# Performance work log

Measured on AMD Instinct MI355X. Metric: run time of the kernel, lower is better.

Reference implementation:

```python
import jax, jax.numpy as jnp
import numpy as np

S = 100                     # MC weight samples
B = 128                     # batch
CONV1 = (100, 20, 1, 5, 5)  # (S, Cout, Cin, kh, kw)
CONV2 = (100, 50, 20, 5, 5)
AFF1 = (100, 500, 800)      # (S, out, in)
AFF2 = (100, 10, 500)
W_OFF = np.cumsum([0, 500, 25000, 400000, 5000])
B_OFF = np.cumsum([0, 20, 50, 500, 10])
NW, NB = 430500, 580


def _softplus(r):
    return jnp.log1p(jnp.exp(r))  # sigma_T(rho) = log(1 + exp(rho))


def _conv(h, w, b):
    # h: (B, S or 1, Cin, H, W); w: (S, Cout, Cin, kh, kw); b: (S, Cout)
    def one(xs, ws):  # xs: (B,Cin,H,W), ws: (Cout,Cin,kh,kw)
        return jax.lax.conv_general_dilated(xs, ws, (1, 1), 'VALID')
    if h.shape[1] == 1:  # shared input broadcast over samples (first layer)
        out = jax.vmap(one, in_axes=(None, 0), out_axes=1)(h[:, 0], w)
    else:
        out = jax.vmap(one, in_axes=(1, 0), out_axes=1)(h, w)
    return out + b[None, :, :, None, None]  # (B,S,Cout,H',W')


def _maxpool(h):  # 2x2 stride-2 over trailing spatial dims
    return jax.lax.reduce_window(h, -jnp.inf, jax.lax.max,
                                 (1, 1, 1, 2, 2), (1, 1, 1, 2, 2), 'VALID')


def setup_inputs() -> dict:
    key = jax.random.key(0)
    ks = jax.random.split(key, 4)
    x = jax.random.normal(ks[0], (B, 1, 28, 28), dtype=jnp.float32)
    e = jax.random.normal(ks[1], (S, NW + NB), dtype=jnp.float32)
    mu_w = jax.random.normal(ks[2], (NW,), dtype=jnp.float32) * 0.05
    rho_w = jnp.ones((NW,), dtype=jnp.float32) * 0.5
    mu_b = jax.random.normal(ks[3], (NB,), dtype=jnp.float32) * 0.05
    rho_b = jnp.ones((NB,), dtype=jnp.float32) * 0.5
    return {"x": x, "e": e, "mu_w": mu_w, "rho_w": rho_w,
            "mu_b": mu_b, "rho_b": rho_b}


def reference(x, e, mu_w, rho_w, mu_b, rho_b):
    # reparameterized per-sample weights: (S, NW) and (S, NB)
    w = mu_w + _softplus(rho_w) * e[:, :NW]
    b = mu_b + _softplus(rho_b) * e[:, NW:]

    h = x[:, None]  # (B,1,1,28,28): singleton MC dim broadcasts
    # conv1 + relu + pool
    h = _conv(h, w[:, W_OFF[0]:W_OFF[1]].reshape(CONV1), b[:, B_OFF[0]:B_OFF[1]])
    h = _maxpool(jax.nn.relu(h))                     # (B,S,20,12,12)
    # conv2 + relu + pool
    h = _conv(h, w[:, W_OFF[1]:W_OFF[2]].reshape(CONV2), b[:, B_OFF[1]:B_OFF[2]])
    h = _maxpool(jax.nn.relu(h))                     # (B,S,50,4,4)
    h = h.reshape(h.shape[0], h.shape[1], -1)        # (B,S,800)
    # aff1 + relu
    w3 = w[:, W_OFF[2]:W_OFF[3]].reshape(AFF1)
    h = jax.nn.relu(jnp.einsum('bsi,soi->bso', h, w3) + b[None, :, B_OFF[2]:B_OFF[3]])
    # aff2 + log_softmax
    w4 = w[:, W_OFF[3]:W_OFF[4]].reshape(AFF2)
    h = jnp.einsum('bsi,soi->bso', h, w4) + b[None, :, B_OFF[3]:B_OFF[4]]
    h = jax.nn.log_softmax(h, axis=-1)               # (B,S,10)
    return h.mean(axis=1)                            # eval path: mean over MC samples
```

## Files before the change

kernel.cpp:

```cpp
#include <hip/hip_runtime.h>
#include <math.h>

#define Sn 100
#define Bn 128
#define NWc 430500
#define EWc 431080

typedef __attribute__((ext_vector_type(8)))  short bhalf8;
typedef __attribute__((ext_vector_type(16))) float fx16;

__device__ __forceinline__ float sp_f(float r){
    return fmaxf(r, 0.f) + log1pf(__expf(-fabsf(r)));
}
__device__ __forceinline__ ushort bfr(float f){
    union { float f; uint u; } c; c.f = f;
    uint r = (c.u + 0x7FFFu + ((c.u >> 16) & 1u)) >> 16;
    return (ushort)r;
}

__global__ void k00_sp(const float* __restrict__ rho_w, const float* __restrict__ rho_b,
                       float* __restrict__ sp_all){
    int i = blockIdx.x * blockDim.x + threadIdx.x;
    if (i < NWc)      sp_all[i] = sp_f(rho_w[i]);
    else if (i < EWc) sp_all[i] = sp_f(rho_b[i - NWc]);
}

__global__ __launch_bounds__(256) void k0_w3t(const float* __restrict__ e,
        const float* __restrict__ mu_w, const float* __restrict__ sp_all,
        ushort* __restrict__ w3){
    __shared__ __align__(16) ushort ls[20*808];
    int oc = blockIdx.x;
    int s  = blockIdx.y;
    int o0 = oc * 20;
    int tid = threadIdx.x;
    const float* eb = e + (size_t)s*EWc + 25500 + (size_t)o0*800;
    const float* mb = mu_w   + 25500 + (size_t)o0*800;
    const float* pb = sp_all + 25500 + (size_t)o0*800;
    #pragma unroll 4
    for (int j = tid; j < 4000; j += 256){
        int o = j / 200, k4 = j - o*200;
        float4 ev = *(const float4*)(eb + j*4);
        float4 mv = *(const float4*)(mb + j*4);
        float4 sv = *(const float4*)(pb + j*4);
        ushort4 t;
        t.x = bfr(fmaf(sv.x, ev.x, mv.x));
        t.y = bfr(fmaf(sv.y, ev.y, mv.y));
        t.z = bfr(fmaf(sv.z, ev.z, mv.z));
        t.w = bfr(fmaf(sv.w, ev.w, mv.w));
        *(ushort4*)&ls[o*808 + k4*4] = t;
    }
    __syncthreads();
    if (tid < 200){
        int kt = tid >> 3, l8 = tid & 7;
        ushort* wb = w3 + (size_t)s*400000 + kt*16000 + o0*32;
        #pragma unroll
        for (int it = 0; it < 10; ++it){
            int idx = it*8 + l8;
            int o = idx >> 2, kp = (idx & 3)*8;
            uint4 v = *(const uint4*)&ls[o*808 + kt*32 + kp];
            *(uint4*)(wb + idx*8) = v;
        }
    }
}

__global__ void k0_small(const float* __restrict__ e, const float* __restrict__ mu_w,
                       const float* __restrict__ sp_all, const float* __restrict__ mu_b,
                       float* __restrict__ w1, ushort* __restrict__ w2r,
                       float* __restrict__ w4, float* __restrict__ ball){
    const int per = 31080;
    int idx = blockIdx.x * blockDim.x + threadIdx.x;
    if (idx >= Sn * per) return;
    int s = idx / per, j = idx % per;
    if (j < 500){
        float v = fmaf(sp_all[j], e[(size_t)s*EWc + j], mu_w[j]);
        w1[s*500 + j] = v;
    } else if (j < 25500){
        int g = j;
        float v = fmaf(sp_all[g], e[(size_t)s*EWc + g], mu_w[g]);
        int j2 = j - 500;
        int oc = j2 / 500, rem = j2 % 500;
        int ic = rem / 25, kk = rem % 25;
        w2r[(size_t)s*51200 + (kk*64 + oc)*32 + ic] = bfr(v);
    } else if (j < 30500){
        int g = 425500 + (j - 25500);
        float v = fmaf(sp_all[g], e[(size_t)s*EWc + g], mu_w[g]);
        w4[s*5000 + (j - 25500)] = v;
    } else {
        int k = j - 30500;
        float v = fmaf(sp_all[NWc + k], e[(size_t)s*EWc + NWc + k], mu_b[k]);
        ball[s*580 + k] = v;
    }
}

__global__ __launch_bounds__(256, 2) void k1_conv1(const float* __restrict__ x,
        const float* __restrict__ w1, const float* __restrict__ ball,
        ushort* __restrict__ h1p){
    __shared__ __align__(16) float xs[784];
    __shared__ __align__(16) float w1s[500];
    __shared__ float b1s[20];
    __shared__ __align__(16) ushort ots[2880];
    int bid = blockIdx.x;
    int s = bid / Bn, b = bid % Bn;
    int tid = threadIdx.x;
    for (int i = tid; i < 784; i += 256) xs[i] = x[b*784 + i];
    for (int i = tid; i < 500; i += 256) w1s[i] = w1[s*500 + i];
    if (tid < 20) b1s[tid] = ball[s*580 + tid];
    __syncthreads();
    if (tid < 240){
        int c = tid / 12, y = tid % 12;

        float acc0[24], acc1[24];
        #pragma unroll
        for (int i = 0; i < 24; ++i){ acc0[i] = 0.f; acc1[i] = 0.f; }

        #pragma unroll
        for (int ky = 0; ky < 5; ++ky){
            float rlo[28], rhi[28];
            const float* plo = &xs[(2*y + ky) * 28];
            const float* phi = &xs[(2*y + ky + 1) * 28];
            #pragma unroll
            for (int cc = 0; cc < 28; cc += 4){
                float4 v0 = *(const float4*)(plo + cc);
                rlo[cc] = v0.x; rlo[cc+1] = v0.y; rlo[cc+2] = v0.z; rlo[cc+3] = v0.w;
                float4 v1 = *(const float4*)(phi + cc);
                rhi[cc] = v1.x; rhi[cc+1] = v1.y; rhi[cc+2] = v1.z; rhi[cc+3] = v1.w;
            }
            #pragma unroll
            for (int kx = 0; kx < 5; ++kx){
                float wv = w1s[c*25 + ky*5 + kx];
                #pragma unroll
                for (int cx = 0; cx < 24; ++cx){
                    acc0[cx] = fmaf(rlo[cx + kx], wv, acc0[cx]);
                    acc1[cx] = fmaf(rhi[cx + kx], wv, acc1[cx]);
                }
            }
        }
        float bias = b1s[c];
        #pragma unroll
        for (int px = 0; px < 12; ++px){
            float m = fmaxf(fmaxf(acc0[2*px], acc0[2*px+1]),
                            fmaxf(acc1[2*px], acc1[2*px+1]));
            ots[(y*12 + px)*20 + c] = bfr(fmaxf(m + bias, 0.f));
        }
    }
    __syncthreads();
    const uint* o32 = (const uint*)ots;
    uint* g32 = (uint*)(h1p + (s*Bn + b)*2880);
    for (int j = tid; j < 1440; j += 256) g32[j] = o32[j];
}

#define ICS 40
__global__ __launch_bounds__(256, 3) void k2_direct(const ushort* __restrict__ h1p,
        const ushort* __restrict__ w2r, const float* __restrict__ ball,
        ushort* __restrict__ h2p){
    __shared__ __align__(16) ushort img[4*144*ICS];
    int bid = blockIdx.x;
    int s = bid >> 5, g = bid & 31;
    int tid = threadIdx.x;
    const uint* g32 = (const uint*)(h1p + (size_t)(s*Bn + g*4)*2880);
    uint* l32 = (uint*)img;
    for (int j = tid; j < 5760; j += 256){
        int im = j / 1440, r = j - im*1440;
        int p = r / 10, u = r - p*10;
        l32[im*2880 + p*20 + u] = g32[j];
    }
    for (int j = tid; j < 3456; j += 256){
        int im = j / 864, r = j - im*864;
        int p = r / 6, u = 10 + (r - p*6);
        l32[im*2880 + p*20 + u] = 0u;
    }
    __syncthreads();

    int wv = tid >> 6, l = tid & 63;
    int l31 = l & 31, q = l >> 5;
    const ushort* imgw = img + wv*5760;
    int pixb0 = ((l31      ) >> 3)*12 + (l31 & 7);
    int pixb1 = ((l31 + 32 ) >> 3)*12 + (l31 & 7);
    const ushort* wb0 = w2r + (size_t)(s*25)*2048 + (l31     )*32;
    const ushort* wb1 = w2r + (size_t)(s*25)*2048 + (l31 + 32)*32;
    fx16 acc00 = (fx16)0.f, acc01 = (fx16)0.f, acc10 = (fx16)0.f, acc11 = (fx16)0.f;

    #pragma unroll 1
    for (int kk = 0; kk < 25; ++kk){
        int ky = kk / 5, kx = kk - ky*5;
        int poff = ky*12 + kx;
        #pragma unroll
        for (int ics = 0; ics < 2; ++ics){
            bhalf8 a0 = *(const bhalf8*)(imgw + (pixb0 + poff)*ICS + ics*16 + q*8);
            bhalf8 a1 = *(const bhalf8*)(imgw + (pixb1 + poff)*ICS + ics*16 + q*8);
            bhalf8 b0 = *(const bhalf8*)(wb0 + kk*2048 + ics*16 + q*8);
            bhalf8 b1 = *(const bhalf8*)(wb1 + kk*2048 + ics*16 + q*8);
            acc00 = __builtin_amdgcn_mfma_f32_32x32x16_bf16(a0, b0, acc00, 0, 0, 0);
            acc01 = __builtin_amdgcn_mfma_f32_32x32x16_bf16(a0, b1, acc01, 0, 0, 0);
            acc10 = __builtin_amdgcn_mfma_f32_32x32x16_bf16(a1, b0, acc10, 0, 0, 0);
            acc11 = __builtin_amdgcn_mfma_f32_32x32x16_bf16(a1, b1, acc11, 0, 0, 0);
        }
    }
    int b = g*4 + wv;
    ushort* dst = h2p + (size_t)s*102400 + (size_t)b*32;
    #pragma unroll
    for (int nt = 0; nt < 2; ++nt){
        int oc = nt*32 + l31;
        if (oc >= 50) continue;
        float bias = ball[s*580 + 20 + oc];
        #pragma unroll
        for (int mt = 0; mt < 2; ++mt){
            fx16 a;
            if (nt == 0) a = mt ? acc10 : acc00;
            else         a = mt ? acc11 : acc01;
            #pragma unroll
            for (int gp = 0; gp < 2; ++gp){
                float p0 = fmaxf(fmaxf(a[8*gp+0], a[8*gp+1]), fmaxf(a[8*gp+4], a[8*gp+5]));
                float p1 = fmaxf(fmaxf(a[8*gp+2], a[8*gp+3]), fmaxf(a[8*gp+6], a[8*gp+7]));
                p0 = fmaxf(p0 + bias, 0.f);
                p1 = fmaxf(p1 + bias, 0.f);
                int py = mt*2 + gp;
                int i  = oc*16 + py*4 + 2*q;
                uint pk = (uint)bfr(p0) | ((uint)bfr(p1) << 16);
                *(uint*)(dst + (i >> 5)*4096 + (i & 31)) = pk;
            }
        }
    }
}

__global__ __launch_bounds__(256) void k3_mfma(const ushort* __restrict__ h2p,
        const ushort* __restrict__ w3, const float* __restrict__ ball,
        float* __restrict__ h3){
    __shared__ __align__(16) ushort As[128*ICS];
    __shared__ __align__(16) ushort Bsh[64*ICS];
    int bid = blockIdx.x;
    int s = bid >> 3, nblk = bid & 7;
    int o0 = nblk * 64;
    int tid = threadIdx.x;
    int wv = tid >> 6, l = tid & 63, l31 = l & 31, q = l >> 5;
    int wm = wv >> 1, wn = wv & 1;
    fx16 acc0 = (fx16)0.f, acc1 = (fx16)0.f;
    int rr = tid >> 2, rk = (tid & 3)*8;
    const ushort* Abase = h2p + (size_t)s*102400;
    const ushort* Bbase = w3  + (size_t)s*400000 + (size_t)o0*32;
    bool bvalid = (o0 + rr) < 500;
    const uint4 z4 = make_uint4(0u,0u,0u,0u);

    uint4 ar0, ar1, br;
    ar0 = *(const uint4*)(Abase + rr*32 + rk);
    ar1 = *(const uint4*)(Abase + (rr + 64)*32 + rk);
    br  = bvalid ? *(const uint4*)(Bbase + rr*32 + rk) : z4;

    for (int kt = 0; kt < 25; ++kt){
        __syncthreads();
        *(uint4*)&As[rr*ICS + rk]        = ar0;
        *(uint4*)&As[(rr + 64)*ICS + rk] = ar1;
        *(uint4*)&Bsh[rr*ICS + rk]       = br;
        __syncthreads();
        if (kt < 24){
            ar0 = *(const uint4*)(Abase + (kt+1)*4096 + rr*32 + rk);
            ar1 = *(const uint4*)(Abase + (kt+1)*4096 + (rr + 64)*32 + rk);
            br  = bvalid ? *(const uint4*)(Bbase + (kt+1)*16000 + rr*32 + rk) : z4;
        }
        #pragma unroll
        for (int ks = 0; ks < 2; ++ks){
            bhalf8 a0 = *(const bhalf8*)&As[(wm*64      + l31)*ICS + ks*16 + q*8];
            bhalf8 a1 = *(const bhalf8*)&As[(wm*64 + 32 + l31)*ICS + ks*16 + q*8];
            bhalf8 bb = *(const bhalf8*)&Bsh[(wn*32 + l31)*ICS + ks*16 + q*8];
            acc0 = __builtin_amdgcn_mfma_f32_32x32x16_bf16(a0, bb, acc0, 0, 0, 0);
            acc1 = __builtin_amdgcn_mfma_f32_32x32x16_bf16(a1, bb, acc1, 0, 0, 0);
        }
    }
    int o = o0 + wn*32 + l31;
    if (o < 500){
        float bias = ball[s*580 + 70 + o];
        #pragma unroll
        for (int mt = 0; mt < 2; ++mt){
            fx16 a = mt ? acc1 : acc0;
            #pragma unroll
            for (int reg = 0; reg < 16; ++reg){
                int row = (reg & 3) + 8*(reg >> 2) + 4*q;
                int b = wm*64 + mt*32 + row;
                h3[(size_t)(s*Bn + b)*500 + o] = fmaxf(a[reg] + bias, 0.f);
            }
        }
    }
}

__global__ __launch_bounds__(256) void k4a(const float* __restrict__ h3,
        const float* __restrict__ w4, const float* __restrict__ ball,
        float* __restrict__ lsw){
    int wv = threadIdx.x >> 6, lane = threadIdx.x & 63;
    int p = blockIdx.x*4 + wv;
    int s = p / Bn;
    const float* hp = &h3[(size_t)p*500];
    const float* wp = &w4[(size_t)s*5000];
    float part[10];
    #pragma unroll
    for (int o = 0; o < 10; ++o) part[o] = 0.f;
    for (int i = lane; i < 500; i += 64){
        float hv = hp[i];
        #pragma unroll
        for (int o = 0; o < 10; ++o)
            part[o] = fmaf(hv, wp[o*500 + i], part[o]);
    }
    #pragma unroll
    for (int o = 0; o < 10; ++o){
        #pragma unroll
        for (int d = 1; d < 64; d <<= 1)
            part[o] += __shfl_xor(part[o], d);
    }
    float v[10]; float m = -INFINITY;
    #pragma unroll
    for (int o = 0; o < 10; ++o){
        v[o] = part[o] + ball[s*580 + 570 + o];
        m = fmaxf(m, v[o]);
    }
    float sum = 0.f;
    #pragma unroll
    for (int o = 0; o < 10; ++o) sum += __expf(v[o] - m);
    float lse = m + __logf(sum);
    if (lane == 0){
        #pragma unroll
        for (int o = 0; o < 10; ++o) lsw[p*10 + o] = v[o] - lse;
    }
}

__global__ void k4b(const float* __restrict__ lsw, float* __restrict__ outp){
    int j = blockIdx.x * blockDim.x + threadIdx.x;
    if (j >= Bn*10) return;
    int b = j / 10, o = j % 10;
    float acc = 0.f;
    for (int s2 = 0; s2 < Sn; ++s2) acc += lsw[(s2*Bn + b)*10 + o];
    outp[j] = acc * (1.f / (float)Sn);
}

extern "C" void kernel_launch(void* const* d_in, const int* in_sizes, int n_in,
                              void* d_out, int out_size, void* d_ws, size_t ws_size,
                              hipStream_t stream){
    const float* x     = (const float*)d_in[0];
    const float* e     = (const float*)d_in[1];
    const float* mu_w  = (const float*)d_in[2];
    const float* rho_w = (const float*)d_in[3];
    const float* mu_b  = (const float*)d_in[4];
    const float* rho_b = (const float*)d_in[5];
    float* ws   = (float*)d_ws;
    float* w1     = ws;
    float* w4     = w1 + 50000;
    float* ball   = w4 + 500000;
    float* h3     = ball + 58000;
    float* lsw    = h3 + 6400000;
    float* sp_all = lsw + 128000;
    ushort* h1p = (ushort*)(sp_all + 431080);
    ushort* h2p = h1p + 36864000;
    ushort* w2r = h2p + 10240000;
    ushort* w3  = w2r + 5120000;
    float* outp = (float*)d_out;

    hipMemsetAsync(w2r, 0, (size_t)Sn*51200*2, stream);
    k00_sp   <<<(EWc + 255)/256, 256, 0, stream>>>(rho_w, rho_b, sp_all);
    k0_w3t   <<<dim3(25, Sn), 256, 0, stream>>>(e, mu_w, sp_all, w3);
    k0_small <<<(Sn*31080 + 255)/256, 256, 0, stream>>>(e, mu_w, sp_all, mu_b, w1, w2r, w4, ball);
    k1_conv1 <<<Sn*Bn, 256, 0, stream>>>(x, w1, ball, h1p);
    k2_direct<<<Sn*32, 256, 0, stream>>>(h1p, w2r, ball, h2p);
    k3_mfma  <<<Sn*8, 256, 0, stream>>>(h2p, w3, ball, h3);
    k4a      <<<3200, 256, 0, stream>>>(h3, w4, ball, lsw);
    k4b      <<<(Bn*10 + 255)/256, 256, 0, stream>>>(lsw, outp);
}
```

Baseline: 555.3 us.

## Swizzle conv2 LDS image layout, prefetch weights, raise occupancy

```diff
diff --git a/kernel.cpp b/kernel.cpp
--- a/kernel.cpp
+++ b/kernel.cpp
@@ -149,11 +149,10 @@
     for (int j = tid; j < 1440; j += 256) g32[j] = o32[j];
 }
 
-#define ICS 40
-__global__ __launch_bounds__(256, 3) void k2_direct(const ushort* __restrict__ h1p,
+__global__ __launch_bounds__(256, 4) void k2_direct(const ushort* __restrict__ h1p,
         const ushort* __restrict__ w2r, const float* __restrict__ ball,
         ushort* __restrict__ h2p){
-    __shared__ __align__(16) ushort img[4*144*ICS];
+    __shared__ __align__(16) ushort img[4*4608];
     int bid = blockIdx.x;
     int s = bid >> 5, g = bid & 31;
     int tid = threadIdx.x;
@@ -162,39 +161,57 @@
     for (int j = tid; j < 5760; j += 256){
         int im = j / 1440, r = j - im*1440;
         int p = r / 10, u = r - p*10;
-        l32[im*2880 + p*20 + u] = g32[j];
+        l32[im*2304 + ((p*16 + u) ^ ((p & 7) << 2))] = g32[j];
     }
     for (int j = tid; j < 3456; j += 256){
         int im = j / 864, r = j - im*864;
         int p = r / 6, u = 10 + (r - p*6);
-        l32[im*2880 + p*20 + u] = 0u;
+        l32[im*2304 + ((p*16 + u) ^ ((p & 7) << 2))] = 0u;
     }
     __syncthreads();
 
     int wv = tid >> 6, l = tid & 63;
     int l31 = l & 31, q = l >> 5;
-    const ushort* imgw = img + wv*5760;
+    const ushort* imgw = img + wv*4608;
     int pixb0 = ((l31      ) >> 3)*12 + (l31 & 7);
     int pixb1 = ((l31 + 32 ) >> 3)*12 + (l31 & 7);
-    const ushort* wb0 = w2r + (size_t)(s*25)*2048 + (l31     )*32;
-    const ushort* wb1 = w2r + (size_t)(s*25)*2048 + (l31 + 32)*32;
+    const ushort* wb0 = w2r + (size_t)(s*25)*2048 + (l31     )*32 + q*8;
+    const ushort* wb1 = w2r + (size_t)(s*25)*2048 + (l31 + 32)*32 + q*8;
     fx16 acc00 = (fx16)0.f, acc01 = (fx16)0.f, acc10 = (fx16)0.f, acc11 = (fx16)0.f;
+
+    bhalf8 b0c = *(const bhalf8*)(wb0);
+    bhalf8 b1c = *(const bhalf8*)(wb1);
+    bhalf8 b2c = *(const bhalf8*)(wb0 + 16);
+    bhalf8 b3c = *(const bhalf8*)(wb1 + 16);
 
     #pragma unroll 1
     for (int kk = 0; kk < 25; ++kk){
+        int kn = (kk < 24) ? (kk + 1) : 24;
+        bhalf8 b0n = *(const bhalf8*)(wb0 + kn*2048);
+        bhalf8 b1n = *(const bhalf8*)(wb1 + kn*2048);
+        bhalf8 b2n = *(const bhalf8*)(wb0 + kn*2048 + 16);
+        bhalf8 b3n = *(const bhalf8*)(wb1 + kn*2048 + 16);
+
         int ky = kk / 5, kx = kk - ky*5;
         int poff = ky*12 + kx;
-        #pragma unroll
-        for (int ics = 0; ics < 2; ++ics){
-            bhalf8 a0 = *(const bhalf8*)(imgw + (pixb0 + poff)*ICS + ics*16 + q*8);
-            bhalf8 a1 = *(const bhalf8*)(imgw + (pixb1 + poff)*ICS + ics*16 + q*8);
-            bhalf8 b0 = *(const bhalf8*)(wb0 + kk*2048 + ics*16 + q*8);
-            bhalf8 b1 = *(const bhalf8*)(wb1 + kk*2048 + ics*16 + q*8);
-            acc00 = __builtin_amdgcn_mfma_f32_32x32x16_bf16(a0, b0, acc00, 0, 0, 0);
-            acc01 = __builtin_amdgcn_mfma_f32_32x32x16_bf16(a0, b1, acc01, 0, 0, 0);
-            acc10 = __builtin_amdgcn_mfma_f32_32x32x16_bf16(a1, b0, acc10, 0, 0, 0);
-            acc11 = __builtin_amdgcn_mfma_f32_32x32x16_bf16(a1, b1, acc11, 0, 0, 0);
-        }
+        int p0 = pixb0 + poff, p1 = pixb1 + poff;
+        int sw0 = (p0 & 7) << 3, sw1 = (p1 & 7) << 3;
+
+        bhalf8 a00 = *(const bhalf8*)(imgw + ((p0*32 +      q*8) ^ sw0));
+        bhalf8 a10 = *(const bhalf8*)(imgw + ((p1*32 +      q*8) ^ sw1));
+        acc00 = __builtin_amdgcn_mfma_f32_32x32x16_bf16(a00, b0c, acc00, 0, 0, 0);
+        acc01 = __builtin_amdgcn_mfma_f32_32x32x16_bf16(a00, b1c, acc01, 0, 0, 0);
+        acc10 = __builtin_amdgcn_mfma_f32_32x32x16_bf16(a10, b0c, acc10, 0, 0, 0);
+        acc11 = __builtin_amdgcn_mfma_f32_32x32x16_bf16(a10, b1c, acc11, 0, 0, 0);
+
+        bhalf8 a01 = *(const bhalf8*)(imgw + ((p0*32 + 16 + q*8) ^ sw0));
+        bhalf8 a11 = *(const bhalf8*)(imgw + ((p1*32 + 16 + q*8) ^ sw1));
+        acc00 = __builtin_amdgcn_mfma_f32_32x32x16_bf16(a01, b2c, acc00, 0, 0, 0);
+        acc01 = __builtin_amdgcn_mfma_f32_32x32x16_bf16(a01, b3c, acc01, 0, 0, 0);
+        acc10 = __builtin_amdgcn_mfma_f32_32x32x16_bf16(a11, b2c, acc10, 0, 0, 0);
+        acc11 = __builtin_amdgcn_mfma_f32_32x32x16_bf16(a11, b3c, acc11, 0, 0, 0);
+
+        b0c = b0n; b1c = b1n; b2c = b2n; b3c = b3n;
     }
     int b = g*4 + wv;
     ushort* dst = h2p + (size_t)s*102400 + (size_t)b*32;
@@ -223,6 +240,7 @@
     }
 }
 
+#define ICS 40
 __global__ __launch_bounds__(256) void k3_mfma(const ushort* __restrict__ h2p,
         const ushort* __restrict__ w3, const float* __restrict__ ball,
         float* __restrict__ h3){
```

Result: no change. 551.3 us (-0.7%).
